# Optimization experiments

Hardware: AMD Instinct MI355X
Metric: run time of the kernel (lower is better)

The kernel has to match this reference:

```python
import jax, jax.numpy as jnp
import numpy as np

HIDDEN = 2048
N_HEADS = 16
N_KV = 4
HEAD_DIM = 128
EPS = 1e-6
B, S = 2, 2048


def rms_norm(x, w, eps=EPS):
    xf = x.astype(jnp.float32)
    var = jnp.mean(xf * xf, axis=-1, keepdims=True)
    return (w * (xf * jax.lax.rsqrt(var + eps))).astype(x.dtype)


def rotate_half(x):
    half = x.shape[-1] // 2
    return jnp.concatenate([-x[..., half:], x[..., :half]], axis=-1)


def setup_inputs() -> dict:
    key = jax.random.key(0)
    ks = jax.random.split(key, 9)
    inv_freq = 1.0 / (10000.0 ** (np.arange(0, HEAD_DIM, 2) / HEAD_DIM))
    ang = np.arange(S)[:, None] * inv_freq[None, :]
    ang = np.concatenate([ang, ang], axis=-1)  # [S, HEAD_DIM]
    return {
        "hidden_states": jax.random.normal(ks[0], (B, S, HIDDEN), jnp.float32),
        "cos": jnp.asarray(np.cos(ang), jnp.float32),
        "sin": jnp.asarray(np.sin(ang), jnp.float32),
        "Wq": jax.random.normal(ks[1], (HIDDEN, N_HEADS * HEAD_DIM), jnp.float32) * 0.02,
        "Wk": jax.random.normal(ks[2], (HIDDEN, N_KV * HEAD_DIM), jnp.float32) * 0.02,
        "Wv": jax.random.normal(ks[3], (HIDDEN, N_KV * HEAD_DIM), jnp.float32) * 0.02,
        "Wo": jax.random.normal(ks[4], (N_HEADS * HEAD_DIM, HIDDEN), jnp.float32) * 0.02,
        "q_norm_w": jnp.ones((HEAD_DIM,), jnp.float32),
        "k_norm_w": jnp.ones((HEAD_DIM,), jnp.float32),
    }


def reference(hidden_states, cos, sin, Wq, Wk, Wv, Wo, q_norm_w, k_norm_w):
    b, s, _ = hidden_states.shape
    n_rep = N_HEADS // N_KV
    scaling = HEAD_DIM ** -0.5

    q = (hidden_states @ Wq).reshape(b, s, N_HEADS, HEAD_DIM)
    k = (hidden_states @ Wk).reshape(b, s, N_KV, HEAD_DIM)
    v = (hidden_states @ Wv).reshape(b, s, N_KV, HEAD_DIM)

    q = rms_norm(q, q_norm_w)
    k = rms_norm(k, k_norm_w)

    q = q.transpose(0, 2, 1, 3)  # [b, h, s, d]
    k = k.transpose(0, 2, 1, 3)  # [b, kv, s, d]
    v = v.transpose(0, 2, 1, 3)

    c = cos[None, None]  # [1,1,s,d]
    si = sin[None, None]
    q = q * c + rotate_half(q) * si
    k = k * c + rotate_half(k) * si

    # repeat kv heads to match query heads
    k = jnp.repeat(k, n_rep, axis=1)
    v = jnp.repeat(v, n_rep, axis=1)

    scores = jnp.einsum("bhqd,bhkd->bhqk", q, k) * scaling
    causal = jnp.triu(jnp.full((s, s), -jnp.inf, jnp.float32), k=1)
    scores = scores + causal
    attn = jax.nn.softmax(scores.astype(jnp.float32), axis=-1).astype(q.dtype)

    out = jnp.einsum("bhqk,bhkd->bhqd", attn, v)
    out = out.transpose(0, 2, 1, 3).reshape(b, s, N_HEADS * HEAD_DIM)
    return out @ Wo
```

## Files before the change

### kernel.cpp

```cpp
#include <hip/hip_runtime.h>

typedef float floatx4 __attribute__((ext_vector_type(4)));
typedef short short8 __attribute__((ext_vector_type(8)));

#define HIDDEN 2048
#define NH 16
#define NKV 4
#define HD 128
#define NB 2
#define SEQ 2048
#define MT (NB * SEQ)
#define NQKV 3072

__device__ __forceinline__ unsigned short f2bf(float x) {
  union { float f; unsigned u; } v; v.f = x;
  unsigned r = v.u + 0x7FFFu + ((v.u >> 16) & 1u);
  return (unsigned short)(r >> 16);
}

__device__ __forceinline__ unsigned int cvt_pk_bf16(float lo, float hi) {
  unsigned int r;
  asm("v_cvt_pk_bf16_f32 %0, %1, %2" : "=v"(r) : "v"(lo), "v"(hi));
  return r;
}

__global__ void cast_bf16_kernel(const float* __restrict__ in,
                                 unsigned short* __restrict__ out, int n4) {
  int i = blockIdx.x * 256 + threadIdx.x;
  if (i >= n4) return;
  float4 v = ((const float4*)in)[i];
  ushort4 o;
  o.x = f2bf(v.x); o.y = f2bf(v.y); o.z = f2bf(v.z); o.w = f2bf(v.w);
  ((ushort4*)out)[i] = o;
}

__global__ void wtrans_kernel(const float* __restrict__ Wq,
                              const float* __restrict__ Wk,
                              const float* __restrict__ Wv,
                              const float* __restrict__ Wo,
                              unsigned short* __restrict__ wqkvt,
                              unsigned short* __restrict__ wot) {
  __shared__ float tile[32][33];
  int z = blockIdx.z;
  int nt = blockIdx.x * 32;
  int k0 = blockIdx.y * 32;
  const float* src;
  unsigned short* dst;
  int Nd, scol0, drow0;
  if (z == 0) {
    src = Wq; Nd = 2048; scol0 = nt; drow0 = nt; dst = wqkvt;
  } else if (z == 1) {
    src = Wo; Nd = 2048; scol0 = nt; drow0 = nt; dst = wot;
  } else {
    if (nt >= 1024) return;
    Nd = 512; dst = wqkvt; drow0 = 2048 + nt;
    if (nt < 512) { src = Wk; scol0 = nt; }
    else          { src = Wv; scol0 = nt - 512; }
  }
  int tx = threadIdx.x, ty = threadIdx.y;
  for (int i = 0; i < 32; i += 8)
    tile[ty + i][tx] = src[(size_t)(k0 + ty + i) * Nd + scol0 + tx];
  __syncthreads();
  for (int i = 0; i < 32; i += 8)
    dst[(size_t)(drow0 + ty + i) * HIDDEN + k0 + tx] = f2bf(tile[tx][ty + i]);
}

__global__ __launch_bounds__(256, 3)
void gemm_bf16_kernel(const unsigned short* __restrict__ A,
                      const unsigned short* __restrict__ Bt,
                      float* __restrict__ C, int M, int N, int K) {
  __shared__ unsigned short As[128 * 32];
  __shared__ unsigned short Bs[128 * 32];
  const int tid = threadIdx.x;
  const int wave = tid >> 6, lane = tid & 63;
  const int quad = lane >> 4, l16 = lane & 15;
  const int m0 = blockIdx.x * 128, n0 = blockIdx.y * 128;
  const int wm = (wave >> 1) * 64, wn = (wave & 1) * 64;
  const int srow = lane >> 2;
  const int scol = (lane & 3) * 8;

  floatx4 acc[4][4] = {};

  for (int kt = 0; kt < K; kt += 32) {
    __syncthreads();
#pragma unroll
    for (int t = 0; t < 2; ++t) {
      int q = wave * 2 + t;
      int row = q * 16 + srow;
      __builtin_amdgcn_global_load_lds(
          (const __attribute__((address_space(1))) unsigned int*)&A[(size_t)(m0 + row) * K + kt + scol],
          (__attribute__((address_space(3))) unsigned int*)&As[q * 16 * 32],
          16, 0, 0);
      __builtin_amdgcn_global_load_lds(
          (const __attribute__((address_space(1))) unsigned int*)&Bt[(size_t)(n0 + row) * K + kt + scol],
          (__attribute__((address_space(3))) unsigned int*)&Bs[q * 16 * 32],
          16, 0, 0);
    }
    __syncthreads();
    short8 af[4], bf[4];
#pragma unroll
    for (int i = 0; i < 4; i++)
      af[i] = *(const short8*)&As[(wm + i * 16 + l16) * 32 + quad * 8];
#pragma unroll
    for (int j = 0; j < 4; j++)
      bf[j] = *(const short8*)&Bs[(wn + j * 16 + l16) * 32 + quad * 8];
#pragma unroll
    for (int i = 0; i < 4; i++)
#pragma unroll
      for (int j = 0; j < 4; j++)
        acc[i][j] = __builtin_amdgcn_mfma_f32_16x16x32_bf16(af[i], bf[j], acc[i][j], 0, 0, 0);
  }
#pragma unroll
  for (int i = 0; i < 4; i++) {
    int row = m0 + wm + i * 16 + quad * 4;
#pragma unroll
    for (int j = 0; j < 4; j++) {
      int col = n0 + wn + j * 16 + l16;
#pragma unroll
      for (int r = 0; r < 4; r++)
        C[(size_t)(row + r) * N + col] = acc[i][j][r];
    }
  }
}

__global__ __launch_bounds__(256, 3)
void gemm_qkv_kernel(const unsigned short* __restrict__ A,
                     const unsigned short* __restrict__ Bt,
                     const float* __restrict__ qw,
                     const float* __restrict__ kw,
                     const float* __restrict__ cosb,
                     const float* __restrict__ sinb,
                     unsigned short* __restrict__ Qb,
                     unsigned short* __restrict__ Kbb,
                     unsigned short* __restrict__ Vt) {
  __shared__ __align__(16) unsigned short As[128 * 32];
  __shared__ __align__(16) unsigned short Bs[128 * 32];
  __shared__ __align__(16) float pscr[4 * 64 * 20];
  __shared__ float pssq[2][128];
  const int tid = threadIdx.x;
  const int wave = tid >> 6, lane = tid & 63;
  const int quad = lane >> 4, l16 = lane & 15;
  const int m0 = blockIdx.x * 128, n0 = blockIdx.y * 128;
  const int wm = (wave >> 1) * 64, wn = (wave & 1) * 64;
  const int srow = lane >> 2;
  const int scol = (lane & 3) * 8;

  floatx4 acc[4][4] = {};

  for (int kt = 0; kt < HIDDEN; kt += 32) {
    __syncthreads();
#pragma unroll
    for (int t = 0; t < 2; ++t) {
      int q = wave * 2 + t;
      int row = q * 16 + srow;
      __builtin_amdgcn_global_load_lds(
          (const __attribute__((address_space(1))) unsigned int*)&A[(size_t)(m0 + row) * HIDDEN + kt + scol],
          (__attribute__((address_space(3))) unsigned int*)&As[q * 16 * 32],
          16, 0, 0);
      __builtin_amdgcn_global_load_lds(
          (const __attribute__((address_space(1))) unsigned int*)&Bt[(size_t)(n0 + row) * HIDDEN + kt + scol],
          (__attribute__((address_space(3))) unsigned int*)&Bs[q * 16 * 32],
          16, 0, 0);
    }
    __syncthreads();
    short8 af[4], bf[4];
#pragma unroll
    for (int i = 0; i < 4; i++)
      af[i] = *(const short8*)&As[(wm + i * 16 + l16) * 32 + quad * 8];
#pragma unroll
    for (int j = 0; j < 4; j++)
      bf[j] = *(const short8*)&Bs[(wn + j * 16 + l16) * 32 + quad * 8];
#pragma unroll
    for (int i = 0; i < 4; i++)
#pragma unroll
      for (int j = 0; j < 4; j++)
        acc[i][j] = __builtin_amdgcn_mfma_f32_16x16x32_bf16(af[i], bf[j], acc[i][j], 0, 0, 0);
  }

  const int head = n0 >> 7;
  if (head >= NH + NKV) {
    const int kv = head - (NH + NKV);
#pragma unroll
    for (int i = 0; i < 4; ++i) {
      int m = m0 + wm + i * 16 + quad * 4;
      int b = m >> 11, sbase = m & (SEQ - 1);
#pragma unroll
      for (int j = 0; j < 4; ++j) {
        int d = wn + j * 16 + l16;
        ushort4 pk;
        pk.x = f2bf(acc[i][j][0]); pk.y = f2bf(acc[i][j][1]);
        pk.z = f2bf(acc[i][j][2]); pk.w = f2bf(acc[i][j][3]);
        *(ushort4*)&Vt[((size_t)(b * NKV + kv) * HD + d) * SEQ + sbase] = pk;
      }
    }
    return;
  }

  const float* w = (head < NH) ? qw : kw;
  float wown[4], wpar[4];
#pragma unroll
  for (int j = 0; j < 4; ++j) {
    wown[j] = w[wn + j * 16 + l16];
    wpar[j] = w[(wn ^ 64) + j * 16 + l16];
  }
#pragma unroll
  for (int i = 0; i < 4; ++i) {
    float sq[4];
#pragma unroll
    for (int r = 0; r < 4; ++r) {
      float s2 = acc[i][0][r] * acc[i][0][r] + acc[i][1][r] * acc[i][1][r] +
                 acc[i][2][r] * acc[i][2][r] + acc[i][3][r] * acc[i][3][r];
#pragma unroll
      for (int off = 1; off < 16; off <<= 1) s2 += __shfl_xor(s2, off, 64);
      sq[r] = s2;
    }
    if (l16 == 0)
      *(float4*)&pssq[wn >> 6][wm + i * 16 + quad * 4] = make_float4(sq[0], sq[1], sq[2], sq[3]);
#pragma unroll
    for (int j = 0; j < 4; ++j)
      *(float4*)&pscr[(wave * 64 + j * 16 + l16) * 20 + quad * 4] = *(float4*)&acc[i][j];
    __syncthreads();
    float4 oss = *(const float4*)&pssq[(wn >> 6) ^ 1][wm + i * 16 + quad * 4];
    float rr[4];
    rr[0] = rsqrtf((sq[0] + oss.x) * (1.0f / 128.0f) + 1e-6f);
    rr[1] = rsqrtf((sq[1] + oss.y) * (1.0f / 128.0f) + 1e-6f);
    rr[2] = rsqrtf((sq[2] + oss.z) * (1.0f / 128.0f) + 1e-6f);
    rr[3] = rsqrtf((sq[3] + oss.w) * (1.0f / 128.0f) + 1e-6f);
    int mbase = m0 + wm + i * 16 + quad * 4;
    int b = mbase >> 11, sbase = mbase & (SEQ - 1);
#pragma unroll
    for (int j = 0; j < 4; ++j) {
      float4 par = *(const float4*)&pscr[((wave ^ 1) * 64 + j * 16 + l16) * 20 + quad * 4];
      float pr[4] = {par.x, par.y, par.z, par.w};
      int d = wn + j * 16 + l16;
      unsigned short* dst = (head < NH)
          ? Qb + ((size_t)(b * NH + head) * SEQ + sbase) * HD + d
          : Kbb + ((size_t)(b * NKV + (head - NH)) * SEQ + sbase) * HD + d;
#pragma unroll
      for (int r = 0; r < 4; ++r) {
        int s = sbase + r;
        float c = cosb[s * HD + d], sn = sinb[s * HD + d];
        float xo = acc[i][j][r] * rr[r] * wown[j];
        float xp = pr[r] * rr[r] * wpar[j];
        float out = (wn == 0) ? (xo * c - xp * sn) : (xo * c + xp * sn);
        dst[(size_t)r * HD] = f2bf(out);
      }
    }
    __syncthreads();
  }
}


__device__ __forceinline__ void stage_rows(const unsigned short* gbase, int rowstride,
                                           unsigned short* lds, int wave, int quad,
                                           int s_cx, int s_hb) {
#pragma unroll
  for (int i = 0; i < 8; ++i) {
    const int row = i * 16 + wave * 4 + quad;
    const int sck = s_cx ^ (((2 * i + s_hb) & 3) << 2);
    __builtin_amdgcn_global_load_lds(
        (const __attribute__((address_space(1))) unsigned int*)(gbase + (size_t)row * rowstride + sck * 8),
        (__attribute__((address_space(3))) unsigned int*)(lds + (i * 4 + wave) * 512),
        16, 0, 0);
  }
}

__global__ __launch_bounds__(256, 2)
void attn_kernel(const unsigned short* __restrict__ Q,
                 const unsigned short* __restrict__ Kb,
                 const unsigned short* __restrict__ Vt,
                 unsigned short* __restrict__ O) {
  __shared__ __align__(16) unsigned short KVs[2][128 * 128];
  const int tid = threadIdx.x;
  const int wave = tid >> 6, lane = tid & 63;
  const int quad = lane >> 4, l16 = lane & 15;
  const int l3 = l16 & 3, s3 = l16 >> 3, s2 = (l16 >> 2) & 1;
  const int bh = blockIdx.x & 31;
  const int pr = blockIdx.x >> 5;
  const int b = bh >> 4, h = bh & 15, kvh = h >> 2;

  const int s_cx = (lane & 15) ^ quad;
  const int s_hb = wave >> 1;
  const int krbase = 16 * s3 + 8 * s2 + l3;
  const int f_k = l3 | ((2 * s3 + s2) << 2);
  const int kvqb = 16 * (quad >> 1) + 8 * (quad & 1);
  const int qsw = (lane & 48) | (quad << 2);
  const float CS = 0.08838834764831845f;

  const unsigned short* Kg0 = Kb + (size_t)((b * NKV + kvh) * SEQ) * HD;
  const unsigned short* Vg0 = Vt + (size_t)((b * NKV + kvh) * HD) * SEQ;

  int p = 0;
#pragma unroll 1
  for (int seg = 0; seg < 2; ++seg) {
    const int qt = seg ? pr : (31 - pr);
    const int q0 = qt * 64;
    const int nkt = (qt >> 1) + 1;
    const int qglob = q0 + wave * 16 + l16;

    const unsigned short* Qg = Q + (size_t)((b * NH + h) * SEQ + q0) * HD;
    short8 qf[4];
#pragma unroll
    for (int ks = 0; ks < 4; ++ks)
      qf[ks] = *(const short8*)&Qg[(size_t)(wave * 16 + l16) * HD + ks * 32 + quad * 8];

    floatx4 oacc[8] = {};
    float mrow = -1e30f, lrow = 0.f;

    stage_rows(Kg0, 128, KVs[p], wave, quad, s_cx, s_hb);
    __syncthreads();

    for (int kt = 0; kt < nkt; ++kt) {
      const unsigned short* KVp = KVs[p];
      floatx4 sc[8] = {};
#pragma unroll
      for (int ks = 0; ks < 4; ++ks) {
        const int cko = ((ks * 4 + quad) ^ f_k) * 8;
#pragma unroll
        for (int j = 0; j < 8; ++j) {
          const short8 kf = *(const short8*)&KVp[(krbase + 32 * (j >> 1) + 4 * (j & 1)) * 128 + cko];
          sc[j] = __builtin_amdgcn_mfma_f32_16x16x32_bf16(kf, qf[ks], sc[j], 0, 0, 0);
        }
      }
      __syncthreads();
      stage_rows(Vg0 + kt * 128, SEQ, KVs[p], wave, quad, s_cx, s_hb);
      if (kt + 1 < nkt)
        stage_rows(Kg0 + (size_t)(kt + 1) * 128 * HD, 128, KVs[p ^ 1], wave, quad, s_cx, s_hb);

      if (kt == nkt - 1) {
#pragma unroll
        for (int j = 0; j < 8; ++j) {
          const int kvj = kt * 128 + 32 * (j >> 1) + 4 * (j & 1) + kvqb;
#pragma unroll
          for (int r = 0; r < 4; ++r)
            if (kvj + r > qglob) sc[j][r] = -1e30f;
        }
      }
      float mx = -1e30f;
#pragma unroll
      for (int j = 0; j < 8; ++j)
        mx = fmaxf(mx, fmaxf(fmaxf(sc[j][0], sc[j][1]), fmaxf(sc[j][2], sc[j][3])));
      mx = fmaxf(mx, __shfl_xor(mx, 16, 64));
      mx = fmaxf(mx, __shfl_xor(mx, 32, 64));
      if (!__all(mx <= mrow + 62.0f)) {
        const float mnew = fmaxf(mrow, mx);
        const float al = __expf((mrow - mnew) * CS);
        mrow = mnew;
        lrow *= al;
#pragma unroll
        for (int r = 0; r < 4; ++r) {
          const float ar = __shfl(al, qsw + r, 64);
#pragma unroll
          for (int t = 0; t < 8; ++t) oacc[t][r] *= ar;
        }
      }
      const float mc = mrow * CS;
      float rs = 0.f;
#pragma unroll
      for (int j = 0; j < 8; ++j)
#pragma unroll
        for (int r = 0; r < 4; ++r) {
          const float pe = __expf(sc[j][r] * CS - mc);
          sc[j][r] = pe;
          rs += pe;
        }
      rs += __shfl_xor(rs, 16, 64);
      rs += __shfl_xor(rs, 32, 64);
      lrow += rs;

      unsigned int pk[8][2];
#pragma unroll
      for (int j = 0; j < 8; ++j) {
        pk[j][0] = cvt_pk_bf16(sc[j][0], sc[j][1]);
        pk[j][1] = cvt_pk_bf16(sc[j][2], sc[j][3]);
      }
      __syncthreads();
#pragma unroll
      for (int ks = 0; ks < 4; ++ks) {
        union { unsigned int u[4]; short8 s; } au;
        au.u[0] = pk[2 * ks][0];     au.u[1] = pk[2 * ks][1];
        au.u[2] = pk[2 * ks + 1][0]; au.u[3] = pk[2 * ks + 1][1];
#pragma unroll
        for (int t = 0; t < 8; ++t) {
          const int fv = l3 | (((2 * t + s3) & 3) << 2);
          const short8 vf = *(const short8*)&KVp[(t * 16 + l16) * 128 + (((ks * 4 + quad) ^ fv) * 8)];
          oacc[t] = __builtin_amdgcn_mfma_f32_16x16x32_bf16(au.s, vf, oacc[t], 0, 0, 0);
        }
      }
      p ^= 1;
    }
    float li[4];
#pragma unroll
    for (int r = 0; r < 4; ++r) li[r] = 1.0f / __shfl(lrow, qsw + r, 64);
#pragma unroll
    for (int t = 0; t < 8; ++t) {
      const int col = h * HD + t * 16 + l16;
#pragma unroll
      for (int r = 0; r < 4; ++r) {
        const int row = q0 + wave * 16 + quad * 4 + r;
        O[(size_t)(b * SEQ + row) * (NH * HD) + col] = f2bf(oacc[t][r] * li[r]);
      }
    }
  }
}

extern "C" void kernel_launch(void* const* d_in, const int* in_sizes, int n_in,
                              void* d_out, int out_size, void* d_ws, size_t ws_size,
                              hipStream_t stream) {
  const float* hidden = (const float*)d_in[0];
  const float* cosb   = (const float*)d_in[1];
  const float* sinb   = (const float*)d_in[2];
  const float* Wq     = (const float*)d_in[3];
  const float* Wk     = (const float*)d_in[4];
  const float* Wv     = (const float*)d_in[5];
  const float* Wo     = (const float*)d_in[6];
  const float* qw     = (const float*)d_in[7];
  const float* kw     = (const float*)d_in[8];
  (void)in_sizes; (void)n_in; (void)out_size; (void)ws_size;

  char* ws = (char*)d_ws;
  size_t off = 0;
  auto alloc = [&](size_t n) { char* p = ws + off; off += (n + 255) & ~(size_t)255; return p; };

  unsigned short* hb    = (unsigned short*)alloc((size_t)MT * HIDDEN * 2);
  unsigned short* wqkvt = (unsigned short*)alloc((size_t)NQKV * HIDDEN * 2);
  unsigned short* wot   = (unsigned short*)alloc((size_t)2048 * 2048 * 2);
  unsigned short* Qb  = (unsigned short*)alloc((size_t)MT * 2048 * 2);
  unsigned short* Kbb = (unsigned short*)alloc((size_t)MT * 512 * 2);
  unsigned short* Vtb = (unsigned short*)alloc((size_t)MT * 512 * 2);
  unsigned short* Ob  = (unsigned short*)alloc((size_t)MT * 2048 * 2);

  cast_bf16_kernel<<<(MT * HIDDEN / 4) / 256, 256, 0, stream>>>(hidden, hb, MT * HIDDEN / 4);
  dim3 tb(32, 8);
  wtrans_kernel<<<dim3(64, 64, 3), tb, 0, stream>>>(Wq, Wk, Wv, Wo, wqkvt, wot);

  gemm_qkv_kernel<<<dim3(MT / 128, NQKV / 128), 256, 0, stream>>>(
      hb, wqkvt, qw, kw, cosb, sinb, Qb, Kbb, Vtb);

  attn_kernel<<<512, 256, 0, stream>>>(Qb, Kbb, Vtb, Ob);

  gemm_bf16_kernel<<<dim3(MT / 128, 16), 256, 0, stream>>>(Ob, wot, (float*)d_out, MT, 2048, 2048);
}
```

Before: 294.5 us.

## Rewrite QKV and output GEMMs as 256-tile double-buffered 8-wave pipelined kernels

Replaces both projection GEMMs with 512-thread kernels using larger 256x256 (QKV) and 256x128 (O) tiles, a K-step of 64, and a double-buffered LDS pipeline. The pipeline uses XOR-swizzled layouts, explicit vmcnt/lgkmcnt waits, sched barriers and setprio to overlap global-to-LDS loads with MFMA work. The fused RMSnorm/RoPE epilogue is remapped to the new wave layout and reuses the dynamic LDS. The cost targeted is the single-buffered, sync-heavy small-tile loop. In exchange, the large LDS footprint allows only one block per CU and lowers occupancy, and the grids get smaller (e.g. 192 blocks for QKV).

```diff
diff --git a/kernel.cpp b/kernel.cpp
--- a/kernel.cpp
+++ b/kernel.cpp
@@ -11,6 +11,13 @@
 #define SEQ 2048
 #define MT (NB * SEQ)
 #define NQKV 3072
+
+#define MFMA16(a, b, c) __builtin_amdgcn_mfma_f32_16x16x32_bf16(a, b, c, 0, 0, 0)
+#define S_BAR() __builtin_amdgcn_s_barrier()
+#define WAIT_LGKM0() do { asm volatile("s_waitcnt lgkmcnt(0)" ::: "memory"); \
+                          __builtin_amdgcn_sched_barrier(0); } while (0)
+#define WAIT_VM(N) do { asm volatile("s_waitcnt vmcnt(" #N ")" ::: "memory"); \
+                        __builtin_amdgcn_sched_barrier(0); } while (0)
 
 __device__ __forceinline__ unsigned short f2bf(float x) {
   union { float f; unsigned u; } v; v.f = x;
@@ -65,65 +72,8 @@
     dst[(size_t)(drow0 + ty + i) * HIDDEN + k0 + tx] = f2bf(tile[tx][ty + i]);
 }
 
-__global__ __launch_bounds__(256, 3)
-void gemm_bf16_kernel(const unsigned short* __restrict__ A,
-                      const unsigned short* __restrict__ Bt,
-                      float* __restrict__ C, int M, int N, int K) {
-  __shared__ unsigned short As[128 * 32];
-  __shared__ unsigned short Bs[128 * 32];
-  const int tid = threadIdx.x;
-  const int wave = tid >> 6, lane = tid & 63;
-  const int quad = lane >> 4, l16 = lane & 15;
-  const int m0 = blockIdx.x * 128, n0 = blockIdx.y * 128;
-  const int wm = (wave >> 1) * 64, wn = (wave & 1) * 64;
-  const int srow = lane >> 2;
-  const int scol = (lane & 3) * 8;
-
-  floatx4 acc[4][4] = {};
-
-  for (int kt = 0; kt < K; kt += 32) {
-    __syncthreads();
-#pragma unroll
-    for (int t = 0; t < 2; ++t) {
-      int q = wave * 2 + t;
-      int row = q * 16 + srow;
-      __builtin_amdgcn_global_load_lds(
-          (const __attribute__((address_space(1))) unsigned int*)&A[(size_t)(m0 + row) * K + kt + scol],
-          (__attribute__((address_space(3))) unsigned int*)&As[q * 16 * 32],
-          16, 0, 0);
-      __builtin_amdgcn_global_load_lds(
-          (const __attribute__((address_space(1))) unsigned int*)&Bt[(size_t)(n0 + row) * K + kt + scol],
-          (__attribute__((address_space(3))) unsigned int*)&Bs[q * 16 * 32],
-          16, 0, 0);
-    }
-    __syncthreads();
-    short8 af[4], bf[4];
-#pragma unroll
-    for (int i = 0; i < 4; i++)
-      af[i] = *(const short8*)&As[(wm + i * 16 + l16) * 32 + quad * 8];
-#pragma unroll
-    for (int j = 0; j < 4; j++)
-      bf[j] = *(const short8*)&Bs[(wn + j * 16 + l16) * 32 + quad * 8];
-#pragma unroll
-    for (int i = 0; i < 4; i++)
-#pragma unroll
-      for (int j = 0; j < 4; j++)
-        acc[i][j] = __builtin_amdgcn_mfma_f32_16x16x32_bf16(af[i], bf[j], acc[i][j], 0, 0, 0);
-  }
-#pragma unroll
-  for (int i = 0; i < 4; i++) {
-    int row = m0 + wm + i * 16 + quad * 4;
-#pragma unroll
-    for (int j = 0; j < 4; j++) {
-      int col = n0 + wn + j * 16 + l16;
-#pragma unroll
-      for (int r = 0; r < 4; r++)
-        C[(size_t)(row + r) * N + col] = acc[i][j][r];
-    }
-  }
-}
-
-__global__ __launch_bounds__(256, 3)
+
+__global__ __launch_bounds__(512, 1)
 void gemm_qkv_kernel(const unsigned short* __restrict__ A,
                      const unsigned short* __restrict__ Bt,
                      const float* __restrict__ qw,
@@ -133,60 +83,138 @@
                      unsigned short* __restrict__ Qb,
                      unsigned short* __restrict__ Kbb,
                      unsigned short* __restrict__ Vt) {
-  __shared__ __align__(16) unsigned short As[128 * 32];
-  __shared__ __align__(16) unsigned short Bs[128 * 32];
-  __shared__ __align__(16) float pscr[4 * 64 * 20];
-  __shared__ float pssq[2][128];
+  extern __shared__ __align__(16) char smem[];
   const int tid = threadIdx.x;
   const int wave = tid >> 6, lane = tid & 63;
   const int quad = lane >> 4, l16 = lane & 15;
-  const int m0 = blockIdx.x * 128, n0 = blockIdx.y * 128;
-  const int wm = (wave >> 1) * 64, wn = (wave & 1) * 64;
-  const int srow = lane >> 2;
-  const int scol = (lane & 3) * 8;
-
-  floatx4 acc[4][4] = {};
-
-  for (int kt = 0; kt < HIDDEN; kt += 32) {
-    __syncthreads();
-#pragma unroll
-    for (int t = 0; t < 2; ++t) {
-      int q = wave * 2 + t;
-      int row = q * 16 + srow;
+  const int m0 = blockIdx.x * 256, n0 = blockIdx.y * 256;
+  const int wm = (wave >> 2) * 128, wn = (wave & 3) * 64;
+
+  const int sgrow = wave * 8 + (lane >> 3);
+  const int swzcol = (((lane & 7) ^ ((lane >> 3) & 7)) << 4);
+  const int laneA0 = l16 * 128 + ((quad ^ (l16 & 7)) << 4);
+  const int laneA1 = laneA0 ^ 64;
+
+  auto stageA = [&](int T, int h) {
+    const char* g = (const char*)A + (((size_t)(m0 + h * 128)) * HIDDEN + T * 64) * 2;
+    char* l = smem + (size_t)(((T & 1) * 2 + h) * 16384) + wave * 1024;
+#pragma unroll
+    for (int ii = 0; ii < 2; ++ii) {
+      const char* src = g + (size_t)(ii * 64 + sgrow) * (HIDDEN * 2) + swzcol;
       __builtin_amdgcn_global_load_lds(
-          (const __attribute__((address_space(1))) unsigned int*)&A[(size_t)(m0 + row) * HIDDEN + kt + scol],
-          (__attribute__((address_space(3))) unsigned int*)&As[q * 16 * 32],
-          16, 0, 0);
+          (const __attribute__((address_space(1))) unsigned int*)src,
+          (__attribute__((address_space(3))) unsigned int*)(l + ii * 8192), 16, 0, 0);
+    }
+  };
+  auto stageB = [&](int T, int h) {
+    const char* g = (const char*)Bt + (((size_t)(n0 + h * 128)) * HIDDEN + T * 64) * 2;
+    char* l = smem + 65536 + (size_t)(((T & 1) * 2 + h) * 16384) + wave * 1024;
+#pragma unroll
+    for (int ii = 0; ii < 2; ++ii) {
+      const char* src = g + (size_t)(ii * 64 + sgrow) * (HIDDEN * 2) + swzcol;
       __builtin_amdgcn_global_load_lds(
-          (const __attribute__((address_space(1))) unsigned int*)&Bt[(size_t)(n0 + row) * HIDDEN + kt + scol],
-          (__attribute__((address_space(3))) unsigned int*)&Bs[q * 16 * 32],
-          16, 0, 0);
-    }
-    __syncthreads();
-    short8 af[4], bf[4];
-#pragma unroll
-    for (int i = 0; i < 4; i++)
-      af[i] = *(const short8*)&As[(wm + i * 16 + l16) * 32 + quad * 8];
-#pragma unroll
-    for (int j = 0; j < 4; j++)
-      bf[j] = *(const short8*)&Bs[(wn + j * 16 + l16) * 32 + quad * 8];
-#pragma unroll
-    for (int i = 0; i < 4; i++)
-#pragma unroll
-      for (int j = 0; j < 4; j++)
-        acc[i][j] = __builtin_amdgcn_mfma_f32_16x16x32_bf16(af[i], bf[j], acc[i][j], 0, 0, 0);
-  }
-
-  const int head = n0 >> 7;
-  if (head >= NH + NKV) {
-    const int kv = head - (NH + NKV);
-#pragma unroll
-    for (int i = 0; i < 4; ++i) {
-      int m = m0 + wm + i * 16 + quad * 4;
+          (const __attribute__((address_space(1))) unsigned int*)src,
+          (__attribute__((address_space(3))) unsigned int*)(l + ii * 8192), 16, 0, 0);
+    }
+  };
+
+  floatx4 acc[8][4] = {};
+  short8 a[4][2], bA[2][2], bB[2][2];
+  const int NT = HIDDEN / 64;
+
+  stageA(0, 0); stageA(0, 1); stageB(0, 0); stageB(0, 1);
+  stageB(1, 0); stageB(1, 1);
+  WAIT_VM(4);
+  S_BAR();
+
+#pragma unroll 1
+  for (int Y = 0; Y < NT; ++Y) {
+    const int cb = Y & 1;
+    const char* Ah = smem + (size_t)((cb * 2 + (wave >> 2)) * 16384);
+    const char* Bh = smem + 65536 + (size_t)((cb * 2 + ((wave & 3) >> 1)) * 16384) +
+                     (wn & 64) * 128;
+    if (Y + 1 < NT) stageA(Y + 1, 0);
+#pragma unroll
+    for (int fi = 0; fi < 4; ++fi) {
+      a[fi][0] = *(const short8*)(Ah + fi * 2048 + laneA0);
+      a[fi][1] = *(const short8*)(Ah + fi * 2048 + laneA1);
+    }
+#pragma unroll
+    for (int fj = 0; fj < 2; ++fj) {
+      bA[fj][0] = *(const short8*)(Bh + fj * 2048 + laneA0);
+      bA[fj][1] = *(const short8*)(Bh + fj * 2048 + laneA1);
+    }
+    WAIT_LGKM0();
+    __builtin_amdgcn_s_setprio(1);
+#pragma unroll
+    for (int fi = 0; fi < 4; ++fi)
+#pragma unroll
+      for (int fj = 0; fj < 2; ++fj) {
+        acc[fi][fj] = MFMA16(a[fi][0], bA[fj][0], acc[fi][fj]);
+        acc[fi][fj] = MFMA16(a[fi][1], bA[fj][1], acc[fi][fj]);
+      }
+    __builtin_amdgcn_s_setprio(0);
+    S_BAR();
+    if (Y + 1 < NT) stageA(Y + 1, 1);
+#pragma unroll
+    for (int fj = 0; fj < 2; ++fj) {
+      bB[fj][0] = *(const short8*)(Bh + 4096 + fj * 2048 + laneA0);
+      bB[fj][1] = *(const short8*)(Bh + 4096 + fj * 2048 + laneA1);
+    }
+    WAIT_LGKM0();
+    __builtin_amdgcn_s_setprio(1);
+#pragma unroll
+    for (int fi = 0; fi < 4; ++fi)
+#pragma unroll
+      for (int fj = 0; fj < 2; ++fj) {
+        acc[fi][2 + fj] = MFMA16(a[fi][0], bB[fj][0], acc[fi][2 + fj]);
+        acc[fi][2 + fj] = MFMA16(a[fi][1], bB[fj][1], acc[fi][2 + fj]);
+      }
+    __builtin_amdgcn_s_setprio(0);
+    S_BAR();
+    if (Y + 2 < NT) stageB(Y + 2, 0);
+#pragma unroll
+    for (int fi = 0; fi < 4; ++fi) {
+      a[fi][0] = *(const short8*)(Ah + 8192 + fi * 2048 + laneA0);
+      a[fi][1] = *(const short8*)(Ah + 8192 + fi * 2048 + laneA1);
+    }
+    WAIT_LGKM0();
+    __builtin_amdgcn_s_setprio(1);
+#pragma unroll
+    for (int fi = 0; fi < 4; ++fi)
+#pragma unroll
+      for (int fj = 0; fj < 2; ++fj) {
+        acc[4 + fi][2 + fj] = MFMA16(a[fi][0], bB[fj][0], acc[4 + fi][2 + fj]);
+        acc[4 + fi][2 + fj] = MFMA16(a[fi][1], bB[fj][1], acc[4 + fi][2 + fj]);
+      }
+    __builtin_amdgcn_s_setprio(0);
+    S_BAR();
+    if (Y + 2 < NT) stageB(Y + 2, 1);
+    __builtin_amdgcn_s_setprio(1);
+#pragma unroll
+    for (int fi = 0; fi < 4; ++fi)
+#pragma unroll
+      for (int fj = 0; fj < 2; ++fj) {
+        acc[4 + fi][fj] = MFMA16(a[fi][0], bA[fj][0], acc[4 + fi][fj]);
+        acc[4 + fi][fj] = MFMA16(a[fi][1], bA[fj][1], acc[4 + fi][fj]);
+      }
+    __builtin_amdgcn_s_setprio(0);
+    if (Y + 2 < NT) { WAIT_VM(4); } else { WAIT_VM(0); }
+    S_BAR();
+  }
+
+  const int tileN = blockIdx.y;
+  const int head2 = tileN * 2 + ((wave & 3) >> 1);
+
+  if (tileN >= 10) {
+    const int kv = head2 - (NH + NKV);
+#pragma unroll
+    for (int i = 0; i < 8; ++i) {
+      int m = m0 + wm + (i >> 2) * 64 + (i & 3) * 16 + quad * 4;
       int b = m >> 11, sbase = m & (SEQ - 1);
 #pragma unroll
       for (int j = 0; j < 4; ++j) {
-        int d = wn + j * 16 + l16;
+        int d = (wave & 1) * 64 + (j >> 1) * 32 + (j & 1) * 16 + l16;
         ushort4 pk;
         pk.x = f2bf(acc[i][j][0]); pk.y = f2bf(acc[i][j][1]);
         pk.z = f2bf(acc[i][j][2]); pk.w = f2bf(acc[i][j][3]);
@@ -196,15 +224,18 @@
     return;
   }
 
-  const float* w = (head < NH) ? qw : kw;
+  float* pscr = (float*)smem;
+  float* pssq = (float*)(smem + 8 * 64 * 20 * 4);
+  const float* w = (head2 < NH) ? qw : kw;
   float wown[4], wpar[4];
 #pragma unroll
   for (int j = 0; j < 4; ++j) {
-    wown[j] = w[wn + j * 16 + l16];
-    wpar[j] = w[(wn ^ 64) + j * 16 + l16];
-  }
-#pragma unroll
-  for (int i = 0; i < 4; ++i) {
+    int d = (wave & 1) * 64 + (j >> 1) * 32 + (j & 1) * 16 + l16;
+    wown[j] = w[d];
+    wpar[j] = w[d ^ 64];
+  }
+#pragma unroll 1
+  for (int i = 0; i < 8; ++i) {
     float sq[4];
 #pragma unroll
     for (int r = 0; r < 4; ++r) {
@@ -215,34 +246,34 @@
       sq[r] = s2;
     }
     if (l16 == 0)
-      *(float4*)&pssq[wn >> 6][wm + i * 16 + quad * 4] = make_float4(sq[0], sq[1], sq[2], sq[3]);
+      *(float4*)&pssq[wave * 16 + quad * 4] = make_float4(sq[0], sq[1], sq[2], sq[3]);
 #pragma unroll
     for (int j = 0; j < 4; ++j)
       *(float4*)&pscr[(wave * 64 + j * 16 + l16) * 20 + quad * 4] = *(float4*)&acc[i][j];
     __syncthreads();
-    float4 oss = *(const float4*)&pssq[(wn >> 6) ^ 1][wm + i * 16 + quad * 4];
+    float4 oss = *(const float4*)&pssq[(wave ^ 1) * 16 + quad * 4];
     float rr[4];
     rr[0] = rsqrtf((sq[0] + oss.x) * (1.0f / 128.0f) + 1e-6f);
     rr[1] = rsqrtf((sq[1] + oss.y) * (1.0f / 128.0f) + 1e-6f);
     rr[2] = rsqrtf((sq[2] + oss.z) * (1.0f / 128.0f) + 1e-6f);
     rr[3] = rsqrtf((sq[3] + oss.w) * (1.0f / 128.0f) + 1e-6f);
-    int mbase = m0 + wm + i * 16 + quad * 4;
+    int mbase = m0 + wm + (i >> 2) * 64 + (i & 3) * 16 + quad * 4;
     int b = mbase >> 11, sbase = mbase & (SEQ - 1);
 #pragma unroll
     for (int j = 0; j < 4; ++j) {
       float4 par = *(const float4*)&pscr[((wave ^ 1) * 64 + j * 16 + l16) * 20 + quad * 4];
       float pr[4] = {par.x, par.y, par.z, par.w};
-      int d = wn + j * 16 + l16;
-      unsigned short* dst = (head < NH)
-          ? Qb + ((size_t)(b * NH + head) * SEQ + sbase) * HD + d
-          : Kbb + ((size_t)(b * NKV + (head - NH)) * SEQ + sbase) * HD + d;
+      int d = (wave & 1) * 64 + (j >> 1) * 32 + (j & 1) * 16 + l16;
+      unsigned short* dst = (head2 < NH)
+          ? Qb + ((size_t)(b * NH + head2) * SEQ + sbase) * HD + d
+          : Kbb + ((size_t)(b * NKV + (head2 - NH)) * SEQ + sbase) * HD + d;
 #pragma unroll
       for (int r = 0; r < 4; ++r) {
         int s = sbase + r;
         float c = cosb[s * HD + d], sn = sinb[s * HD + d];
         float xo = acc[i][j][r] * rr[r] * wown[j];
         float xp = pr[r] * rr[r] * wpar[j];
-        float out = (wn == 0) ? (xo * c - xp * sn) : (xo * c + xp * sn);
+        float out = ((wave & 1) == 0) ? (xo * c - xp * sn) : (xo * c + xp * sn);
         dst[(size_t)r * HD] = f2bf(out);
       }
     }
@@ -250,6 +281,125 @@
   }
 }
 
+__global__ __launch_bounds__(512, 1)
+void gemm_o_kernel(const unsigned short* __restrict__ A,
+                   const unsigned short* __restrict__ Bt,
+                   float* __restrict__ C) {
+  extern __shared__ __align__(16) char smem[];
+  const int tid = threadIdx.x;
+  const int wave = tid >> 6, lane = tid & 63;
+  const int quad = lane >> 4, l16 = lane & 15;
+  const int m0 = blockIdx.x * 256, n0 = blockIdx.y * 128;
+  const int wm = (wave >> 2) * 128, wn = (wave & 3) * 32;
+
+  const int sgrow = wave * 8 + (lane >> 3);
+  const int swzcol = (((lane & 7) ^ ((lane >> 3) & 7)) << 4);
+  const int laneA0 = l16 * 128 + ((quad ^ (l16 & 7)) << 4);
+  const int laneA1 = laneA0 ^ 64;
+
+  auto stageA = [&](int T, int h) {
+    const char* g = (const char*)A + (((size_t)(m0 + h * 128)) * HIDDEN + T * 64) * 2;
+    char* l = smem + (size_t)(((T & 1) * 2 + h) * 16384) + wave * 1024;
+#pragma unroll
+    for (int ii = 0; ii < 2; ++ii) {
+      const char* src = g + (size_t)(ii * 64 + sgrow) * (HIDDEN * 2) + swzcol;
+      __builtin_amdgcn_global_load_lds(
+          (const __attribute__((address_space(1))) unsigned int*)src,
+          (__attribute__((address_space(3))) unsigned int*)(l + ii * 8192), 16, 0, 0);
+    }
+  };
+  auto stageB = [&](int T, int h) {
+    const char* g = (const char*)Bt + (((size_t)(n0 + h * 64)) * HIDDEN + T * 64) * 2;
+    char* l = smem + 65536 + (size_t)(((T & 1) * 2 + h) * 8192) + wave * 1024;
+    const char* src = g + (size_t)sgrow * (HIDDEN * 2) + swzcol;
+    __builtin_amdgcn_global_load_lds(
+        (const __attribute__((address_space(1))) unsigned int*)src,
+        (__attribute__((address_space(3))) unsigned int*)l, 16, 0, 0);
+  };
+
+  floatx4 acc[8][2] = {};
+  short8 a[4][2], bAv[2], bBv[2];
+  const int NT = HIDDEN / 64;
+
+  stageA(0, 0); stageA(0, 1); stageB(0, 0); stageB(0, 1);
+  stageB(1, 0); stageB(1, 1);
+  WAIT_VM(2);
+  S_BAR();
+
+#pragma unroll 1
+  for (int Y = 0; Y < NT; ++Y) {
+    const int cb = Y & 1;
+    const char* Ah = smem + (size_t)((cb * 2 + (wave >> 2)) * 16384);
+    const char* Bh = smem + 65536 + (size_t)((cb * 2 + ((wave & 3) >> 1)) * 8192) +
+                     (wn & 32) * 128;
+    if (Y + 1 < NT) stageA(Y + 1, 0);
+#pragma unroll
+    for (int fi = 0; fi < 4; ++fi) {
+      a[fi][0] = *(const short8*)(Ah + fi * 2048 + laneA0);
+      a[fi][1] = *(const short8*)(Ah + fi * 2048 + laneA1);
+    }
+    bAv[0] = *(const short8*)(Bh + laneA0);
+    bAv[1] = *(const short8*)(Bh + laneA1);
+    WAIT_LGKM0();
+    __builtin_amdgcn_s_setprio(1);
+#pragma unroll
+    for (int fi = 0; fi < 4; ++fi) {
+      acc[fi][0] = MFMA16(a[fi][0], bAv[0], acc[fi][0]);
+      acc[fi][0] = MFMA16(a[fi][1], bAv[1], acc[fi][0]);
+    }
+    __builtin_amdgcn_s_setprio(0);
+    S_BAR();
+    if (Y + 1 < NT) stageA(Y + 1, 1);
+    bBv[0] = *(const short8*)(Bh + 2048 + laneA0);
+    bBv[1] = *(const short8*)(Bh + 2048 + laneA1);
+    WAIT_LGKM0();
+    __builtin_amdgcn_s_setprio(1);
+#pragma unroll
+    for (int fi = 0; fi < 4; ++fi) {
+      acc[fi][1] = MFMA16(a[fi][0], bBv[0], acc[fi][1]);
+      acc[fi][1] = MFMA16(a[fi][1], bBv[1], acc[fi][1]);
+    }
+    __builtin_amdgcn_s_setprio(0);
+    S_BAR();
+    if (Y + 2 < NT) stageB(Y + 2, 0);
+#pragma unroll
+    for (int fi = 0; fi < 4; ++fi) {
+      a[fi][0] = *(const short8*)(Ah + 8192 + fi * 2048 + laneA0);
+      a[fi][1] = *(const short8*)(Ah + 8192 + fi * 2048 + laneA1);
+    }
+    WAIT_LGKM0();
+    __builtin_amdgcn_s_setprio(1);
+#pragma unroll
+    for (int fi = 0; fi < 4; ++fi) {
+      acc[4 + fi][1] = MFMA16(a[fi][0], bBv[0], acc[4 + fi][1]);
+      acc[4 + fi][1] = MFMA16(a[fi][1], bBv[1], acc[4 + fi][1]);
+    }
+    __builtin_amdgcn_s_setprio(0);
+    S_BAR();
+    if (Y + 2 < NT) stageB(Y + 2, 1);
+    __builtin_amdgcn_s_setprio(1);
+#pragma unroll
+    for (int fi = 0; fi < 4; ++fi) {
+      acc[4 + fi][0] = MFMA16(a[fi][0], bAv[0], acc[4 + fi][0]);
+      acc[4 + fi][0] = MFMA16(a[fi][1], bAv[1], acc[4 + fi][0]);
+    }
+    __builtin_amdgcn_s_setprio(0);
+    if (Y + 2 < NT) { WAIT_VM(2); } else { WAIT_VM(0); }
+    S_BAR();
+  }
+
+#pragma unroll
+  for (int i = 0; i < 8; ++i) {
+    int row = m0 + wm + (i >> 2) * 64 + (i & 3) * 16 + quad * 4;
+#pragma unroll
+    for (int j = 0; j < 2; ++j) {
+      int col = n0 + wn + j * 16 + l16;
+#pragma unroll
+      for (int r = 0; r < 4; ++r)
+        C[(size_t)(row + r) * 2048 + col] = acc[i][j][r];
+    }
+  }
+}
 
 __device__ __forceinline__ void stage_rows(const unsigned short* gbase, int rowstride,
                                            unsigned short* lds, int wave, int quad,
@@ -430,14 +580,23 @@
   unsigned short* Vtb = (unsigned short*)alloc((size_t)MT * 512 * 2);
   unsigned short* Ob  = (unsigned short*)alloc((size_t)MT * 2048 * 2);
 
+  static bool attr_done = false;
+  if (!attr_done) {
+    hipFuncSetAttribute((const void*)gemm_qkv_kernel,
+                        hipFuncAttributeMaxDynamicSharedMemorySize, 131072);
+    hipFuncSetAttribute((const void*)gemm_o_kernel,
+                        hipFuncAttributeMaxDynamicSharedMemorySize, 98304);
+    attr_done = true;
+  }
+
   cast_bf16_kernel<<<(MT * HIDDEN / 4) / 256, 256, 0, stream>>>(hidden, hb, MT * HIDDEN / 4);
   dim3 tb(32, 8);
   wtrans_kernel<<<dim3(64, 64, 3), tb, 0, stream>>>(Wq, Wk, Wv, Wo, wqkvt, wot);
 
-  gemm_qkv_kernel<<<dim3(MT / 128, NQKV / 128), 256, 0, stream>>>(
+  gemm_qkv_kernel<<<dim3(MT / 256, NQKV / 256), 512, 131072, stream>>>(
       hb, wqkvt, qw, kw, cosb, sinb, Qb, Kbb, Vtb);
 
   attn_kernel<<<512, 256, 0, stream>>>(Qb, Kbb, Vtb, Ob);
 
-  gemm_bf16_kernel<<<dim3(MT / 128, 16), 256, 0, stream>>>(Ob, wot, (float*)d_out, MT, 2048, 2048);
-}
+  gemm_o_kernel<<<dim3(MT / 256, 2048 / 128), 512, 98304, stream>>>(Ob, wot, (float*)d_out);
+}
```

New measurement: 333.5 us. +13.3%, slower.

## Double GEMM K-tile to 64 with XOR-swizzled LDS and grouped block remapping

Applied to the files above, without the earlier changes.

Both bf16 GEMM kernels (output projection and fused QKV) now stage 64-wide K tiles instead of 32, which halves the barrier count per K. The LDS layout uses an XOR swizzle on 16-byte chunks to avoid bank conflicts on fragment reads, and workgroup IDs are remapped in groups of eight for better L2 locality. The QKV kernel aliases its epilogue scratch onto the staging buffers with an added barrier, which keeps LDS at 32KB. The larger tiles raise LDS use in the plain GEMM, which may affect occupancy.

```diff
diff --git a/kernel.cpp b/kernel.cpp
--- a/kernel.cpp
+++ b/kernel.cpp
@@ -65,50 +65,63 @@
     dst[(size_t)(drow0 + ty + i) * HIDDEN + k0 + tx] = f2bf(tile[tx][ty + i]);
 }
 
+
 __global__ __launch_bounds__(256, 3)
 void gemm_bf16_kernel(const unsigned short* __restrict__ A,
                       const unsigned short* __restrict__ Bt,
                       float* __restrict__ C, int M, int N, int K) {
-  __shared__ unsigned short As[128 * 32];
-  __shared__ unsigned short Bs[128 * 32];
+  __shared__ unsigned short As[128 * 64];
+  __shared__ unsigned short Bs[128 * 64];
   const int tid = threadIdx.x;
   const int wave = tid >> 6, lane = tid & 63;
   const int quad = lane >> 4, l16 = lane & 15;
-  const int m0 = blockIdx.x * 128, n0 = blockIdx.y * 128;
+  const int nwg = gridDim.x * gridDim.y;
+  const int orig = blockIdx.y * gridDim.x + blockIdx.x;
+  const int lin = (orig & 7) * (nwg >> 3) + (orig >> 3);
+  const int bx = lin % gridDim.x, by = lin / gridDim.x;
+  const int m0 = bx * 128, n0 = by * 128;
   const int wm = (wave >> 1) * 64, wn = (wave & 1) * 64;
-  const int srow = lane >> 2;
-  const int scol = (lane & 3) * 8;
+  const int srow8 = lane >> 3;
+  const int scol = (((lane & 7) ^ srow8) * 8);
+  const int rsw = (l16 & 7);
 
   floatx4 acc[4][4] = {};
 
-  for (int kt = 0; kt < K; kt += 32) {
-    __syncthreads();
-#pragma unroll
-    for (int t = 0; t < 2; ++t) {
-      int q = wave * 2 + t;
-      int row = q * 16 + srow;
+  for (int kt = 0; kt < K; kt += 64) {
+    __syncthreads();
+#pragma unroll
+    for (int t = 0; t < 4; ++t) {
+      int row = t * 32 + wave * 8 + srow8;
       __builtin_amdgcn_global_load_lds(
           (const __attribute__((address_space(1))) unsigned int*)&A[(size_t)(m0 + row) * K + kt + scol],
-          (__attribute__((address_space(3))) unsigned int*)&As[q * 16 * 32],
+          (__attribute__((address_space(3))) unsigned int*)&As[(t * 32 + wave * 8) * 64],
           16, 0, 0);
+    }
+#pragma unroll
+    for (int t = 0; t < 4; ++t) {
+      int row = t * 32 + wave * 8 + srow8;
       __builtin_amdgcn_global_load_lds(
           (const __attribute__((address_space(1))) unsigned int*)&Bt[(size_t)(n0 + row) * K + kt + scol],
-          (__attribute__((address_space(3))) unsigned int*)&Bs[q * 16 * 32],
+          (__attribute__((address_space(3))) unsigned int*)&Bs[(t * 32 + wave * 8) * 64],
           16, 0, 0);
     }
     __syncthreads();
-    short8 af[4], bf[4];
-#pragma unroll
-    for (int i = 0; i < 4; i++)
-      af[i] = *(const short8*)&As[(wm + i * 16 + l16) * 32 + quad * 8];
-#pragma unroll
-    for (int j = 0; j < 4; j++)
-      bf[j] = *(const short8*)&Bs[(wn + j * 16 + l16) * 32 + quad * 8];
-#pragma unroll
-    for (int i = 0; i < 4; i++)
+#pragma unroll
+    for (int kk = 0; kk < 2; ++kk) {
+      const int ck = ((kk * 4 + quad) ^ rsw) * 8;
+      short8 af[4], bf[4];
+#pragma unroll
+      for (int i = 0; i < 4; i++)
+        af[i] = *(const short8*)&As[(wm + i * 16 + l16) * 64 + ck];
 #pragma unroll
       for (int j = 0; j < 4; j++)
-        acc[i][j] = __builtin_amdgcn_mfma_f32_16x16x32_bf16(af[i], bf[j], acc[i][j], 0, 0, 0);
+        bf[j] = *(const short8*)&Bs[(wn + j * 16 + l16) * 64 + ck];
+#pragma unroll
+      for (int i = 0; i < 4; i++)
+#pragma unroll
+        for (int j = 0; j < 4; j++)
+          acc[i][j] = __builtin_amdgcn_mfma_f32_16x16x32_bf16(af[i], bf[j], acc[i][j], 0, 0, 0);
+    }
   }
 #pragma unroll
   for (int i = 0; i < 4; i++) {
@@ -133,48 +146,61 @@
                      unsigned short* __restrict__ Qb,
                      unsigned short* __restrict__ Kbb,
                      unsigned short* __restrict__ Vt) {
-  __shared__ __align__(16) unsigned short As[128 * 32];
-  __shared__ __align__(16) unsigned short Bs[128 * 32];
-  __shared__ __align__(16) float pscr[4 * 64 * 20];
-  __shared__ float pssq[2][128];
+  __shared__ __align__(16) char sh[32768];
+  unsigned short* As = (unsigned short*)sh;
+  unsigned short* Bs = (unsigned short*)(sh + 16384);
+  float* pscr = (float*)sh;
+  float* pssq = (float*)(sh + 20480);
   const int tid = threadIdx.x;
   const int wave = tid >> 6, lane = tid & 63;
   const int quad = lane >> 4, l16 = lane & 15;
-  const int m0 = blockIdx.x * 128, n0 = blockIdx.y * 128;
+  const int nwg = gridDim.x * gridDim.y;
+  const int orig = blockIdx.y * gridDim.x + blockIdx.x;
+  const int lin = (orig & 7) * (nwg >> 3) + (orig >> 3);
+  const int bx = lin % gridDim.x, by = lin / gridDim.x;
+  const int m0 = bx * 128, n0 = by * 128;
   const int wm = (wave >> 1) * 64, wn = (wave & 1) * 64;
-  const int srow = lane >> 2;
-  const int scol = (lane & 3) * 8;
+  const int srow8 = lane >> 3;
+  const int scol = (((lane & 7) ^ srow8) * 8);
+  const int rsw = (l16 & 7);
 
   floatx4 acc[4][4] = {};
 
-  for (int kt = 0; kt < HIDDEN; kt += 32) {
-    __syncthreads();
-#pragma unroll
-    for (int t = 0; t < 2; ++t) {
-      int q = wave * 2 + t;
-      int row = q * 16 + srow;
+  for (int kt = 0; kt < HIDDEN; kt += 64) {
+    __syncthreads();
+#pragma unroll
+    for (int t = 0; t < 4; ++t) {
+      int row = t * 32 + wave * 8 + srow8;
       __builtin_amdgcn_global_load_lds(
           (const __attribute__((address_space(1))) unsigned int*)&A[(size_t)(m0 + row) * HIDDEN + kt + scol],
-          (__attribute__((address_space(3))) unsigned int*)&As[q * 16 * 32],
+          (__attribute__((address_space(3))) unsigned int*)&As[(t * 32 + wave * 8) * 64],
           16, 0, 0);
+    }
+#pragma unroll
+    for (int t = 0; t < 4; ++t) {
+      int row = t * 32 + wave * 8 + srow8;
       __builtin_amdgcn_global_load_lds(
           (const __attribute__((address_space(1))) unsigned int*)&Bt[(size_t)(n0 + row) * HIDDEN + kt + scol],
-          (__attribute__((address_space(3))) unsigned int*)&Bs[q * 16 * 32],
+          (__attribute__((address_space(3))) unsigned int*)&Bs[(t * 32 + wave * 8) * 64],
           16, 0, 0);
     }
     __syncthreads();
-    short8 af[4], bf[4];
-#pragma unroll
-    for (int i = 0; i < 4; i++)
-      af[i] = *(const short8*)&As[(wm + i * 16 + l16) * 32 + quad * 8];
-#pragma unroll
-    for (int j = 0; j < 4; j++)
-      bf[j] = *(const short8*)&Bs[(wn + j * 16 + l16) * 32 + quad * 8];
-#pragma unroll
-    for (int i = 0; i < 4; i++)
+#pragma unroll
+    for (int kk = 0; kk < 2; ++kk) {
+      const int ck = ((kk * 4 + quad) ^ rsw) * 8;
+      short8 af[4], bf[4];
+#pragma unroll
+      for (int i = 0; i < 4; i++)
+        af[i] = *(const short8*)&As[(wm + i * 16 + l16) * 64 + ck];
 #pragma unroll
       for (int j = 0; j < 4; j++)
-        acc[i][j] = __builtin_amdgcn_mfma_f32_16x16x32_bf16(af[i], bf[j], acc[i][j], 0, 0, 0);
+        bf[j] = *(const short8*)&Bs[(wn + j * 16 + l16) * 64 + ck];
+#pragma unroll
+      for (int i = 0; i < 4; i++)
+#pragma unroll
+        for (int j = 0; j < 4; j++)
+          acc[i][j] = __builtin_amdgcn_mfma_f32_16x16x32_bf16(af[i], bf[j], acc[i][j], 0, 0, 0);
+    }
   }
 
   const int head = n0 >> 7;
@@ -196,6 +222,7 @@
     return;
   }
 
+  __syncthreads();
   const float* w = (head < NH) ? qw : kw;
   float wown[4], wpar[4];
 #pragma unroll
@@ -215,12 +242,12 @@
       sq[r] = s2;
     }
     if (l16 == 0)
-      *(float4*)&pssq[wn >> 6][wm + i * 16 + quad * 4] = make_float4(sq[0], sq[1], sq[2], sq[3]);
+      *(float4*)&pssq[(wn >> 6) * 128 + wm + i * 16 + quad * 4] = make_float4(sq[0], sq[1], sq[2], sq[3]);
 #pragma unroll
     for (int j = 0; j < 4; ++j)
       *(float4*)&pscr[(wave * 64 + j * 16 + l16) * 20 + quad * 4] = *(float4*)&acc[i][j];
     __syncthreads();
-    float4 oss = *(const float4*)&pssq[(wn >> 6) ^ 1][wm + i * 16 + quad * 4];
+    float4 oss = *(const float4*)&pssq[((wn >> 6) ^ 1) * 128 + wm + i * 16 + quad * 4];
     float rr[4];
     rr[0] = rsqrtf((sq[0] + oss.x) * (1.0f / 128.0f) + 1e-6f);
     rr[1] = rsqrtf((sq[1] + oss.y) * (1.0f / 128.0f) + 1e-6f);
@@ -249,7 +276,6 @@
     __syncthreads();
   }
 }
-
 
 __device__ __forceinline__ void stage_rows(const unsigned short* gbase, int rowstride,
                                            unsigned short* lds, int wave, int quad,
```

New measurement: 292.7 us. No clear change (-0.6%).
